# Optimization experiments

Hardware: AMD Instinct MI355X
Metric: run time of the kernel (lower is better)

## Reference

```python
import jax, jax.numpy as jnp
import numpy as np

D, H, W = 16, 16, 16          # token grid = img_size/patch_size at i_layer=0
NUM_HEADS = 8
DISTANCE = 10.0               # 10 - i_layer


def _local_pattern(d, h, w, distance):
    # faithful to local_nd_pattern: meshgrid (ij), flatten, cdist p=2, < distance
    g = jnp.meshgrid(jnp.arange(d), jnp.arange(h), jnp.arange(w), indexing='ij')
    coords = jnp.stack([c.reshape(-1) for c in g], axis=1).astype(jnp.float32)  # [N,3]
    diff = coords[:, None, :] - coords[None, :, :]                               # [N,N,3]
    dist = jnp.sqrt(jnp.sum(diff * diff, axis=-1))
    return dist < distance                                                       # [N,N] bool


def setup_inputs() -> dict:
    key = jax.random.key(0)
    k1, k2, k3 = jax.random.split(key, 3)
    dim = 256
    x = jax.random.normal(k1, (1, dim, D, H, W), dtype=jnp.float32)
    qkv_w = jax.random.normal(k2, (3 * dim, dim), dtype=jnp.float32) * (dim ** -0.5)
    proj_w = jax.random.normal(k3, (dim, dim), dtype=jnp.float32) * (dim ** -0.5)
    proj_b = jnp.zeros((dim,), dtype=jnp.float32)
    return {"x": x, "qkv_w": qkv_w, "proj_w": proj_w, "proj_b": proj_b}


def reference(x, qkv_w, proj_w, proj_b):
    b, c, d, h, w = x.shape
    n = d * h * w
    hd = c // NUM_HEADS
    mask = _local_pattern(d, h, w, DISTANCE)                  # [N,N] bool

    # b c d h w -> b (dhw) c
    tok = x.reshape(b, c, n).transpose(0, 2, 1)               # [B,N,C]
    qkv = jnp.einsum('bnc,oc->bno', tok, qkv_w)               # [B,N,3C]
    qkv = qkv.reshape(b, n, 3, NUM_HEADS, hd)
    qkv = qkv.transpose(2, 0, 3, 1, 4)                        # [3,B,H,N,hd]
    q, k, v = qkv[0], qkv[1], qkv[2]                          # [B,H,N,hd]

    scale = 1.0 / jnp.sqrt(jnp.asarray(hd, dtype=x.dtype))
    scores = jnp.einsum('bhnd,bhmd->bhnm', q, k) * scale      # [B,H,N,N]
    scores = jnp.where(mask[None, None], scores, -jnp.inf)
    attn = jax.nn.softmax(scores, axis=-1)
    out = jnp.einsum('bhnm,bhmd->bhnd', attn, v)              # [B,H,N,hd]

    out = out.transpose(0, 2, 1, 3).reshape(b, n, c)          # [B,N,C]
    out = jnp.einsum('bnc,oc->bno', out, proj_w) + proj_b
    # b (dhw) c -> b c d h w
    out = out.transpose(0, 2, 1).reshape(b, c, d, h, w)
    return out
```

## Files before the change

### kernel.cpp

```cpp
#include <hip/hip_runtime.h>
#include <hip/hip_bf16.h>

typedef __attribute__((ext_vector_type(8))) short short8;
typedef __attribute__((ext_vector_type(8))) unsigned short ushort8;
typedef __attribute__((ext_vector_type(4))) float floatx4;

#define L2E 1.4426950408889634f

#if __has_builtin(__builtin_amdgcn_exp2f)
#define EXP2(x) __builtin_amdgcn_exp2f(x)
#else
#define EXP2(x) exp2f(x)
#endif
#if __has_builtin(__builtin_amdgcn_rcpf)
#define RCP(x) __builtin_amdgcn_rcpf(x)
#else
#define RCP(x) (1.0f / (x))
#endif

static __device__ __forceinline__ unsigned short f2bf(float f) {
    unsigned int u = __builtin_bit_cast(unsigned int, f);
    u += 0x7fffu + ((u >> 16) & 1u);
    return (unsigned short)(u >> 16);
}
static __device__ __forceinline__ unsigned int pk_bf16(float a, float b) {
    __hip_bfloat162 h2 = __float22bfloat162_rn(make_float2(a, b));
    unsigned int u;
    __builtin_memcpy(&u, &h2, 4);
    return u;
}

__global__ __launch_bounds__(256) void k_qkv(const float* __restrict__ x,
                                             const float* __restrict__ qw,
                                             unsigned short* __restrict__ qm,
                                             unsigned short* __restrict__ km,
                                             unsigned short* __restrict__ vt) {
    __shared__ __align__(16) unsigned short At[64][136];
    __shared__ __align__(16) unsigned short Wt[64][136];
    const int tid = threadIdx.x;
    const int wave = tid >> 6, lane = tid & 63;
    const int l16 = lane & 15, quad = lane >> 4;
    const int m0 = blockIdx.x * 64;
    const int o0 = blockIdx.y * 64;

    floatx4 acc[4] = {};
    for (int rnd = 0; rnd < 2; ++rnd) {
        const int cbase = rnd * 128;
        if (rnd) __syncthreads();
        {
            const int moff = (tid & 3) * 16;
            #pragma unroll
            for (int half = 0; half < 2; ++half) {
                const int c_l = (tid >> 2) + 64 * half;
                const float4* xp = reinterpret_cast<const float4*>(
                    x + (size_t)(cbase + c_l) * 4096 + m0 + moff);
                const float4 f0 = xp[0], f1 = xp[1], f2 = xp[2], f3 = xp[3];
                At[moff +  0][c_l] = f2bf(f0.x); At[moff +  1][c_l] = f2bf(f0.y);
                At[moff +  2][c_l] = f2bf(f0.z); At[moff +  3][c_l] = f2bf(f0.w);
                At[moff +  4][c_l] = f2bf(f1.x); At[moff +  5][c_l] = f2bf(f1.y);
                At[moff +  6][c_l] = f2bf(f1.z); At[moff +  7][c_l] = f2bf(f1.w);
                At[moff +  8][c_l] = f2bf(f2.x); At[moff +  9][c_l] = f2bf(f2.y);
                At[moff + 10][c_l] = f2bf(f2.z); At[moff + 11][c_l] = f2bf(f2.w);
                At[moff + 12][c_l] = f2bf(f3.x); At[moff + 13][c_l] = f2bf(f3.y);
                At[moff + 14][c_l] = f2bf(f3.z); At[moff + 15][c_l] = f2bf(f3.w);
            }
        }
        {
            const int o_l = tid >> 2, cp = (tid & 3) * 32;
            const float4* wp = reinterpret_cast<const float4*>(
                qw + (size_t)(o0 + o_l) * 256 + cbase + cp);
            #pragma unroll
            for (int j = 0; j < 2; ++j) {
                const float4 g0 = wp[4 * j + 0], g1 = wp[4 * j + 1];
                const float4 g2 = wp[4 * j + 2], g3 = wp[4 * j + 3];
                unsigned int u[8];
                u[0] = pk_bf16(g0.x, g0.y); u[1] = pk_bf16(g0.z, g0.w);
                u[2] = pk_bf16(g1.x, g1.y); u[3] = pk_bf16(g1.z, g1.w);
                u[4] = pk_bf16(g2.x, g2.y); u[5] = pk_bf16(g2.z, g2.w);
                u[6] = pk_bf16(g3.x, g3.y); u[7] = pk_bf16(g3.z, g3.w);
                __builtin_memcpy(&Wt[o_l][cp + 16 * j], u, 32);
            }
        }
        __syncthreads();
        #pragma unroll
        for (int cc = 0; cc < 4; ++cc) {
            const int c0 = cc * 32 + quad * 8;
            const short8 a = *reinterpret_cast<const short8*>(&At[wave * 16 + l16][c0]);
            #pragma unroll
            for (int t4 = 0; t4 < 4; ++t4) {
                const short8 b = *reinterpret_cast<const short8*>(&Wt[t4 * 16 + l16][c0]);
                acc[t4] = __builtin_amdgcn_mfma_f32_16x16x32_bf16(a, b, acc[t4], 0, 0, 0);
            }
        }
    }
    const float qscale = 0.17677669529663687f * L2E;
    #pragma unroll
    for (int t4 = 0; t4 < 4; ++t4) {
        #pragma unroll
        for (int r = 0; r < 4; ++r) {
            const int n = m0 + wave * 16 + quad * 4 + r;
            const int o = o0 + t4 * 16 + l16;
            const int s = o >> 8, rem = o & 255, head = rem >> 5, t = rem & 31;
            if (s == 0)       qm[((size_t)head * 4096 + n) * 32 + t] = f2bf(acc[t4][r] * qscale);
            else if (s == 1)  km[((size_t)head * 4096 + n) * 32 + t] = f2bf(acc[t4][r]);
            else              vt[((size_t)head * 32 + t) * 4096 + n] = f2bf(acc[t4][r]);
        }
    }
}

__global__ __launch_bounds__(256, 4) void k_attn(const unsigned short* __restrict__ qm,
                                              const unsigned short* __restrict__ km,
                                              const unsigned short* __restrict__ vt,
                                              unsigned short* __restrict__ ao) {
    const int h   = blockIdx.y;
    const int nq0 = blockIdx.x * 16;
    const int tid = threadIdx.x;
    const int wv  = __builtin_amdgcn_readfirstlane(tid >> 6);
    const int lane = tid & 63;
    const int l16 = lane & 15, quad = lane >> 4;

    __shared__ __align__(16) char smem[4][4608];
    typedef unsigned short ptrow_t[16][72];
    ptrow_t* PTw = reinterpret_cast<ptrow_t*>(smem[wv]);

    const short8 a_q = *reinterpret_cast<const short8*>(
        qm + ((size_t)h * 4096 + nq0 + l16) * 32 + quad * 8);

    const int hq = (nq0 >> 4) & 15, dq = nq0 >> 8;
    float dw2[4];
    #pragma unroll
    for (int r = 0; r < 4; ++r) {
        const float dw = (float)(quad * 4 + r - l16);
        dw2[r] = dw * dw;
    }

    const unsigned short* kmh = km + ((size_t)h << 17) + l16 * 32 + quad * 8;
    const unsigned short* vt0 = vt + ((size_t)(h * 32 + l16) << 12) + quad * 8;
    const unsigned short* vt1 = vt0 + (16 << 12);

    float l_acc = 0.f;
    floatx4 o_acc[2] = {};

    int jt = -1, c = 0;

#define SCAN(J0, THR)                                                     \
    J0 = -1;                                                              \
    while (++jt < 64) {                                                   \
        const int dk = jt >> 2, hk0 = (jt & 3) * 4;                       \
        const int dd = dq - dk;                                           \
        int dh = 0;                                                       \
        if (hq < hk0) dh = hk0 - hq;                                      \
        else if (hq > hk0 + 3) dh = hq - hk0 - 3;                         \
        if (dd * dd + dh * dh >= 100) continue;                           \
        if (((c++) & 3) != wv) continue;                                  \
        J0 = jt * 64;                                                     \
        const int bb = 100 - dd * dd;                                     \
        THR[0] = bb - (hq - hk0) * (hq - hk0);                            \
        THR[1] = bb - (hq - hk0 - 1) * (hq - hk0 - 1);                    \
        THR[2] = bb - (hq - hk0 - 2) * (hq - hk0 - 2);                    \
        THR[3] = bb - (hq - hk0 - 3) * (hq - hk0 - 3);                    \
        break;                                                            \
    }

#define SSTAGE(THR, KB, BUF)                                              \
    {                                                                     \
        _Pragma("unroll")                                                 \
        for (int t4 = 0; t4 < 4; ++t4) {                                  \
            const bool sib = (THR[t4 ^ 1] > 0);                           \
            if (THR[t4] > 0) {                                            \
                const floatx4 sf = __builtin_amdgcn_mfma_f32_16x16x32_bf16( \
                    KB[t4], a_q, (floatx4){0.f, 0.f, 0.f, 0.f}, 0, 0, 0); \
                const float thrf = (float)THR[t4];                        \
                const float p0 = (dw2[0] < thrf) ? EXP2(sf[0]) : 0.f;     \
                const float p1 = (dw2[1] < thrf) ? EXP2(sf[1]) : 0.f;     \
                const float p2 = (dw2[2] < thrf) ? EXP2(sf[2]) : 0.f;     \
                const float p3 = (dw2[3] < thrf) ? EXP2(sf[3]) : 0.f;     \
                l_acc += (p0 + p1) + (p2 + p3);                           \
                unsigned int pair[2];                                     \
                pair[0] = pk_bf16(p0, p1);                                \
                pair[1] = pk_bf16(p2, p3);                                \
                __builtin_memcpy(&PTw[BUF][l16][t4 * 16 + quad * 4], pair, 8); \
            } else if (sib) {                                             \
                const unsigned int zz[2] = {0u, 0u};                      \
                __builtin_memcpy(&PTw[BUF][l16][t4 * 16 + quad * 4], zz, 8); \
            }                                                             \
        }                                                                 \
    }

    int j0p, thrp[4];
    SCAN(j0p, thrp)
    if (j0p >= 0) {
        short8 kprev[4];
        #pragma unroll
        for (int t4 = 0; t4 < 4; ++t4)
            kprev[t4] = *reinterpret_cast<const short8*>(kmh + ((j0p + t4 * 16) << 5));
        SSTAGE(thrp, kprev, 0)
    }

    int j0c, thrc[4];
    SCAN(j0c, thrc)
    short8 kb[4];
    if (j0c >= 0) {
        #pragma unroll
        for (int t4 = 0; t4 < 4; ++t4)
            kb[t4] = *reinterpret_cast<const short8*>(kmh + ((j0c + t4 * 16) << 5));
    }

    int pb = 0;
    while (j0p >= 0) {
        const short8 v00 = *reinterpret_cast<const short8*>(vt0 + j0p);
        const short8 v01 = *reinterpret_cast<const short8*>(vt1 + j0p);
        const short8 v10 = *reinterpret_cast<const short8*>(vt0 + j0p + 32);
        const short8 v11 = *reinterpret_cast<const short8*>(vt1 + j0p + 32);

        if (j0c >= 0) SSTAGE(thrc, kb, pb ^ 1)

        int j0n, thrn[4];
        SCAN(j0n, thrn)
        short8 kn[4];
        if (j0n >= 0) {
            #pragma unroll
            for (int t4 = 0; t4 < 4; ++t4)
                kn[t4] = *reinterpret_cast<const short8*>(kmh + ((j0n + t4 * 16) << 5));
        }

        #pragma unroll
        for (int kt = 0; kt < 2; ++kt) {
            if (thrp[2 * kt] <= 0 && thrp[2 * kt + 1] <= 0) continue;
            const short8 b_p = *reinterpret_cast<const short8*>(
                &PTw[pb][l16][kt * 32 + quad * 8]);
            o_acc[0] = __builtin_amdgcn_mfma_f32_16x16x32_bf16(
                kt ? v10 : v00, b_p, o_acc[0], 0, 0, 0);
            o_acc[1] = __builtin_amdgcn_mfma_f32_16x16x32_bf16(
                kt ? v11 : v01, b_p, o_acc[1], 0, 0, 0);
        }

        j0p = j0c;
        #pragma unroll
        for (int t4 = 0; t4 < 4; ++t4) { thrp[t4] = thrc[t4]; kb[t4] = kn[t4]; thrc[t4] = thrn[t4]; }
        j0c = j0n;
        pb ^= 1;
    }
#undef SSTAGE
#undef SCAN

    float (*obufw)[20] = reinterpret_cast<float(*)[20]>(smem[wv]);
    float* lbufw = reinterpret_cast<float*>(smem[wv] + 2560);

    l_acc += __shfl_xor(l_acc, 16);
    l_acc += __shfl_xor(l_acc, 32);
    if (lane < 16) lbufw[l16] = l_acc;
    #pragma unroll
    for (int tt = 0; tt < 2; ++tt)
        #pragma unroll
        for (int r = 0; r < 4; ++r)
            obufw[tt * 16 + quad * 4 + r][l16] = o_acc[tt][r];
    __syncthreads();

    const int q = tid & 15, d0 = (tid >> 4) * 2;
    float lt = 0.f, oa = 0.f, ob = 0.f;
    #pragma unroll
    for (int w = 0; w < 4; ++w) {
        const float (*obw)[20] = reinterpret_cast<const float(*)[20]>(smem[w]);
        lt += reinterpret_cast<const float*>(smem[w] + 2560)[q];
        oa += obw[d0][q];
        ob += obw[d0 + 1][q];
    }
    const float inv = RCP(lt);
    const unsigned int uo = pk_bf16(oa * inv, ob * inv);
    *reinterpret_cast<unsigned int*>(ao + (size_t)(nq0 + q) * 256 + h * 32 + d0) = uo;
}

__global__ __launch_bounds__(256) void k_proj(const unsigned short* __restrict__ ao,
                                              const float* __restrict__ pw,
                                              const float* __restrict__ pb,
                                              float* __restrict__ out) {
    __shared__ __align__(16) unsigned short Pt[64][264];
    const int tid = threadIdx.x;
    const int wave = tid >> 6, lane = tid & 63;
    const int l16 = lane & 15, quad = lane >> 4;
    const int n0 = blockIdx.x * 64;
    const int m0 = blockIdx.y * 64;

    {
        const int o_l = tid >> 2, cp = (tid & 3) * 64;
        const float4* wp = reinterpret_cast<const float4*>(pw + (size_t)(m0 + o_l) * 256 + cp);
        #pragma unroll
        for (int j = 0; j < 4; ++j) {
            const float4 g0 = wp[4 * j + 0], g1 = wp[4 * j + 1];
            const float4 g2 = wp[4 * j + 2], g3 = wp[4 * j + 3];
            unsigned int u[8];
            u[0] = pk_bf16(g0.x, g0.y); u[1] = pk_bf16(g0.z, g0.w);
            u[2] = pk_bf16(g1.x, g1.y); u[3] = pk_bf16(g1.z, g1.w);
            u[4] = pk_bf16(g2.x, g2.y); u[5] = pk_bf16(g2.z, g2.w);
            u[6] = pk_bf16(g3.x, g3.y); u[7] = pk_bf16(g3.z, g3.w);
            __builtin_memcpy(&Pt[o_l][cp + 16 * j], u, 32);
        }
    }
    __syncthreads();

    floatx4 acc[4] = {};
    #pragma unroll
    for (int cc = 0; cc < 8; ++cc) {
        const int c0 = cc * 32 + quad * 8;
        const short8 a = *reinterpret_cast<const short8*>(&Pt[wave * 16 + l16][c0]);
        #pragma unroll
        for (int t4 = 0; t4 < 4; ++t4) {
            const short8 b = *reinterpret_cast<const short8*>(
                ao + (size_t)(n0 + t4 * 16 + l16) * 256 + c0);
            acc[t4] = __builtin_amdgcn_mfma_f32_16x16x32_bf16(a, b, acc[t4], 0, 0, 0);
        }
    }
    #pragma unroll
    for (int t4 = 0; t4 < 4; ++t4) {
        #pragma unroll
        for (int r = 0; r < 4; ++r) {
            const int o = m0 + wave * 16 + quad * 4 + r;
            const int n = n0 + t4 * 16 + l16;
            out[(size_t)o * 4096 + n] = acc[t4][r] + pb[o];
        }
    }
}

extern "C" void kernel_launch(void* const* d_in, const int* in_sizes, int n_in,
                              void* d_out, int out_size, void* d_ws, size_t ws_size,
                              hipStream_t stream) {
    const float* x      = (const float*)d_in[0];
    const float* qkv_w  = (const float*)d_in[1];
    const float* proj_w = (const float*)d_in[2];
    const float* proj_b = (const float*)d_in[3];
    float* out = (float*)d_out;

    char* B = (char*)d_ws;
    const size_t MB = 1u << 20;
    unsigned short* ao = (unsigned short*)(B);
    unsigned short* qm = (unsigned short*)(B + 2 * MB);
    unsigned short* km = (unsigned short*)(B + 4 * MB);
    unsigned short* vt = (unsigned short*)(B + 6 * MB);

    k_qkv<<<dim3(64, 12), 256, 0, stream>>>(x, qkv_w, qm, km, vt);
    k_attn<<<dim3(256, 8), 256, 0, stream>>>(qm, km, vt, ao);
    k_proj<<<dim3(64, 4), 256, 0, stream>>>(ao, proj_w, proj_b, out);
}
```

Before: 161.1 us.

## Prefetch K and V two tiles ahead with triple-buffered register rotation

The attention loop now issues the V loads together with the K loads for the tile two steps ahead, instead of loading V at the start of the iteration that consumes it. Three named register sets are rotated through an unrolled-by-three loop, so no register copies are needed between iterations. The launch bound's minimum-occupancy argument drops from 4 to 3 to make room for the extra in-flight registers. The aim is to hide global-load latency for V, at the cost of higher register pressure and possibly lower occupancy.

Result: slower. 170.1 us (+5.6%).

```diff
diff --git a/kernel.cpp b/kernel.cpp
--- a/kernel.cpp
+++ b/kernel.cpp
@@ -108,7 +108,7 @@
     }
 }
 
-__global__ __launch_bounds__(256, 4) void k_attn(const unsigned short* __restrict__ qm,
+__global__ __launch_bounds__(256, 3) void k_attn(const unsigned short* __restrict__ qm,
                                               const unsigned short* __restrict__ km,
                                               const unsigned short* __restrict__ vt,
                                               unsigned short* __restrict__ ao) {
@@ -148,7 +148,7 @@
     while (++jt < 64) {                                                   \
         const int dk = jt >> 2, hk0 = (jt & 3) * 4;                       \
         const int dd = dq - dk;                                           \
-        int dh = 0;                                                       \
+        int dh = 0;                                                      \
         if (hq < hk0) dh = hk0 - hq;                                      \
         else if (hq > hk0 + 3) dh = hq - hk0 - 3;                         \
         if (dd * dd + dh * dh >= 100) continue;                           \
@@ -187,60 +187,55 @@
         }                                                                 \
     }
 
-    int j0p, thrp[4];
-    SCAN(j0p, thrp)
-    if (j0p >= 0) {
-        short8 kprev[4];
-        #pragma unroll
-        for (int t4 = 0; t4 < 4; ++t4)
-            kprev[t4] = *reinterpret_cast<const short8*>(kmh + ((j0p + t4 * 16) << 5));
-        SSTAGE(thrp, kprev, 0)
-    }
-
-    int j0c, thrc[4];
-    SCAN(j0c, thrc)
-    short8 kb[4];
-    if (j0c >= 0) {
-        #pragma unroll
-        for (int t4 = 0; t4 < 4; ++t4)
-            kb[t4] = *reinterpret_cast<const short8*>(kmh + ((j0c + t4 * 16) << 5));
-    }
-
+#define KVLOAD(N)                                                         \
+    if (j0_##N >= 0) {                                                    \
+        _Pragma("unroll")                                                 \
+        for (int t4 = 0; t4 < 4; ++t4)                                    \
+            k_##N[t4] = *reinterpret_cast<const short8*>(                 \
+                kmh + ((j0_##N + t4 * 16) << 5));                         \
+        v_##N[0] = *reinterpret_cast<const short8*>(vt0 + j0_##N);        \
+        v_##N[1] = *reinterpret_cast<const short8*>(vt1 + j0_##N);        \
+        v_##N[2] = *reinterpret_cast<const short8*>(vt0 + j0_##N + 32);   \
+        v_##N[3] = *reinterpret_cast<const short8*>(vt1 + j0_##N + 32);   \
+    }
+
+#define BODY(P, C, N)                                                     \
+    if (j0_##P < 0) break;                                                \
+    SCAN(j0_##N, thr_##N)                                                 \
+    KVLOAD(N)                                                             \
+    if (j0_##C >= 0) SSTAGE(thr_##C, k_##C, pb ^ 1)                       \
+    _Pragma("unroll")                                                     \
+    for (int kt = 0; kt < 2; ++kt) {                                      \
+        if (thr_##P[2 * kt] > 0 || thr_##P[2 * kt + 1] > 0) {             \
+            const short8 b_p = *reinterpret_cast<const short8*>(          \
+                &PTw[pb][l16][kt * 32 + quad * 8]);                       \
+            o_acc[0] = __builtin_amdgcn_mfma_f32_16x16x32_bf16(           \
+                v_##P[2 * kt], b_p, o_acc[0], 0, 0, 0);                   \
+            o_acc[1] = __builtin_amdgcn_mfma_f32_16x16x32_bf16(           \
+                v_##P[2 * kt + 1], b_p, o_acc[1], 0, 0, 0);               \
+        }                                                                 \
+    }                                                                     \
+    pb ^= 1;
+
+    int j0_0 = -1, j0_1 = -1, j0_2 = -1;
+    int thr_0[4] = {}, thr_1[4] = {}, thr_2[4] = {};
+    short8 k_0[4] = {}, k_1[4] = {}, k_2[4] = {};
+    short8 v_0[4] = {}, v_1[4] = {}, v_2[4] = {};
     int pb = 0;
-    while (j0p >= 0) {
-        const short8 v00 = *reinterpret_cast<const short8*>(vt0 + j0p);
-        const short8 v01 = *reinterpret_cast<const short8*>(vt1 + j0p);
-        const short8 v10 = *reinterpret_cast<const short8*>(vt0 + j0p + 32);
-        const short8 v11 = *reinterpret_cast<const short8*>(vt1 + j0p + 32);
-
-        if (j0c >= 0) SSTAGE(thrc, kb, pb ^ 1)
-
-        int j0n, thrn[4];
-        SCAN(j0n, thrn)
-        short8 kn[4];
-        if (j0n >= 0) {
-            #pragma unroll
-            for (int t4 = 0; t4 < 4; ++t4)
-                kn[t4] = *reinterpret_cast<const short8*>(kmh + ((j0n + t4 * 16) << 5));
-        }
-
-        #pragma unroll
-        for (int kt = 0; kt < 2; ++kt) {
-            if (thrp[2 * kt] <= 0 && thrp[2 * kt + 1] <= 0) continue;
-            const short8 b_p = *reinterpret_cast<const short8*>(
-                &PTw[pb][l16][kt * 32 + quad * 8]);
-            o_acc[0] = __builtin_amdgcn_mfma_f32_16x16x32_bf16(
-                kt ? v10 : v00, b_p, o_acc[0], 0, 0, 0);
-            o_acc[1] = __builtin_amdgcn_mfma_f32_16x16x32_bf16(
-                kt ? v11 : v01, b_p, o_acc[1], 0, 0, 0);
-        }
-
-        j0p = j0c;
-        #pragma unroll
-        for (int t4 = 0; t4 < 4; ++t4) { thrp[t4] = thrc[t4]; kb[t4] = kn[t4]; thrc[t4] = thrn[t4]; }
-        j0c = j0n;
-        pb ^= 1;
-    }
+
+    SCAN(j0_0, thr_0)
+    KVLOAD(0)
+    if (j0_0 >= 0) SSTAGE(thr_0, k_0, 0)
+    SCAN(j0_1, thr_1)
+    KVLOAD(1)
+
+    for (;;) {
+        BODY(0, 1, 2)
+        BODY(1, 2, 0)
+        BODY(2, 0, 1)
+    }
+#undef BODY
+#undef KVLOAD
 #undef SSTAGE
 #undef SCAN
 
```
